# Optimization experiments

Hardware: AMD Instinct MI355X
Metric: run time of the kernel (lower is better)

The kernel has to match this reference:

```python
import jax, jax.numpy as jnp
import numpy as np

E, H, BLOCK = 1024, 64, 2048

def setup_inputs() -> dict:
    key = jax.random.key(0)
    kx, kk, kq, kv = jax.random.split(key, 4)
    s = 1.0 / np.sqrt(E)
    return {
        "x": jax.random.normal(kx, (16, 2048, E), dtype=jnp.float32),
        "Wk": jax.random.uniform(kk, (E, H), jnp.float32, -s, s),
        "Wq": jax.random.uniform(kq, (E, H), jnp.float32, -s, s),
        "Wv": jax.random.uniform(kv, (E, H), jnp.float32, -s, s),
    }

def reference(x, Wk, Wq, Wv):
    B, T, C = x.shape
    k = x @ Wk  # [B,T,H]
    q = x @ Wq
    v = x @ Wv
    scale = jnp.asarray(H, x.dtype) ** -0.5
    wei = jnp.einsum("bth,bsh->bts", q, k) * scale  # [B,T,T]
    causal = jnp.tril(jnp.ones((T, T), dtype=bool))
    wei = jnp.where(causal, wei, -jnp.inf)
    wei = jax.nn.softmax(wei, axis=-1)
    # dropout is identity in eval mode
    return jnp.einsum("bts,bsh->bth", wei, v)
```

## Files before the change

### kernel.cpp

```cpp
#include <hip/hip_runtime.h>


typedef __bf16 bf16x8 __attribute__((ext_vector_type(8)));
typedef __bf16 bf16x4 __attribute__((ext_vector_type(4)));
typedef float f32x4 __attribute__((ext_vector_type(4)));

constexpr int kE = 1024;
constexpr int kH = 64;
constexpr int kT = 2048;
constexpr int kB = 16;
constexpr int kM = kB * kT;
constexpr float kQScale = 0.125f * 1.44269504088896340736f;

#define MFMA16(a, b, c) __builtin_amdgcn_mfma_f32_16x16x32_bf16((a), (b), (c), 0, 0, 0)

__device__ __forceinline__ void gl_lds16(const void* g, void* l) {
    __builtin_amdgcn_global_load_lds(
        (const __attribute__((address_space(1))) void*)g,
        (__attribute__((address_space(3))) void*)l, 16, 0, 0);
}

__global__ __launch_bounds__(256)
void prep_w(const float* __restrict__ Wq, const float* __restrict__ Wk,
            const float* __restrict__ Wv, __bf16* __restrict__ WbT)
{
    __shared__ float tl[64][65];
    const int mat = blockIdx.x >> 4;
    const int k0 = (blockIdx.x & 15) * 64;
    const float* src = (mat == 0) ? Wq : (mat == 1) ? Wk : Wv;

    const int t = threadIdx.x;
    const int kr = t >> 2;
    const int cg = (t & 3) * 16;
    #pragma unroll
    for (int i = 0; i < 4; ++i) {
        float4 v = *(const float4*)&src[(size_t)(k0 + kr) * kH + cg + 4 * i];
        tl[cg + 4 * i + 0][kr] = v.x;
        tl[cg + 4 * i + 1][kr] = v.y;
        tl[cg + 4 * i + 2][kr] = v.z;
        tl[cg + 4 * i + 3][kr] = v.w;
    }
    __syncthreads();
    const int nl = t >> 2;
    const int kg = (t & 3) * 16;
    bf16x8 o0, o1;
    #pragma unroll
    for (int j = 0; j < 8; ++j) {
        o0[j] = (__bf16)tl[nl][kg + j];
        o1[j] = (__bf16)tl[nl][kg + 8 + j];
    }
    *(bf16x8*)&WbT[(size_t)(mat * 64 + nl) * kE + k0 + kg] = o0;
    *(bf16x8*)&WbT[(size_t)(mat * 64 + nl) * kE + k0 + kg + 8] = o1;
}

__global__ __launch_bounds__(256)
void qkv(const float* __restrict__ x, const __bf16* __restrict__ WbT,
         __bf16* __restrict__ qo, __bf16* __restrict__ ko, __bf16* __restrict__ vT)
{
    __shared__ __align__(16) char Ab[2][8192];
    __shared__ __align__(16) char Bb[2][24576];

    const int t = threadIdx.x;
    const int lane = t & 63;
    const int w = t >> 6;
    const int l15 = lane & 15;
    const int Q = lane >> 4;
    const int row0 = blockIdx.x * 64;

    f32x4 acc[4][3];
    #pragma unroll
    for (int mt = 0; mt < 4; ++mt)
        #pragma unroll
        for (int nt = 0; nt < 3; ++nt) acc[mt][nt] = (f32x4){0.f, 0.f, 0.f, 0.f};

    auto stageB = [&](int p, int k0) {
        #pragma unroll
        for (int i = 0; i < 6; ++i) {
            const int n = (w * 6 + i) * 8 + (lane >> 3);
            const int g = (lane & 7) ^ (lane >> 3);
            gl_lds16(&WbT[(size_t)n * kE + k0 + g * 8],
                     &Bb[p][(w * 6 + i) * 1024]);
        }
    };

    float4 ar[4];
    auto loadA = [&](int k0) {
        #pragma unroll
        for (int j = 0; j < 4; ++j) {
            const int row = w * 16 + j * 4 + (lane >> 4);
            ar[j] = *(const float4*)&x[(size_t)(row0 + row) * kE + k0 + l15 * 4];
        }
    };
    auto writeA = [&](int p) {
        #pragma unroll
        for (int j = 0; j < 4; ++j) {
            const int r = w * 16 + j * 4 + (lane >> 4);
            bf16x4 pk;
            pk[0] = (__bf16)ar[j].x; pk[1] = (__bf16)ar[j].y;
            pk[2] = (__bf16)ar[j].z; pk[3] = (__bf16)ar[j].w;
            *(bf16x4*)&Ab[p][r * 128 + (((l15 >> 1) ^ (r & 7)) * 16) + (l15 & 1) * 8] = pk;
        }
    };

    loadA(0);
    stageB(0, 0);
    writeA(0);
    __syncthreads();

    for (int c = 0; c < 16; ++c) {
        const int p = c & 1;
        if (c < 15) {
            loadA((c + 1) * 64);
            stageB(1 - p, (c + 1) * 64);
        }

        #pragma unroll
        for (int ks = 0; ks < 2; ++ks) {
            bf16x8 a4[4];
            #pragma unroll
            for (int mt = 0; mt < 4; ++mt) {
                const int row = mt * 16 + l15;
                a4[mt] = *(const bf16x8*)
                    &Ab[p][row * 128 + (((ks * 4 + Q) ^ (l15 & 7)) * 16)];
            }
            #pragma unroll
            for (int nt = 0; nt < 3; ++nt) {
                const int n = w * 48 + nt * 16 + l15;
                bf16x8 b = *(const bf16x8*)&Bb[p][n * 128 + (((ks * 4 + Q) ^ (l15 & 7)) * 16)];
                #pragma unroll
                for (int mt = 0; mt < 4; ++mt)
                    acc[mt][nt] = MFMA16(a4[mt], b, acc[mt][nt]);
            }
        }

        if (c < 15) writeA(1 - p);
        __syncthreads();
    }

    const int batch = row0 >> 11;
    const int tr0 = row0 & 2047;
    #pragma unroll
    for (int nt = 0; nt < 3; ++nt) {
        const int col0 = w * 48 + nt * 16;
        const int mat = col0 >> 6;
        const int c = (col0 & 63) + l15;
        if (mat == 2) {
            #pragma unroll
            for (int mt = 0; mt < 4; ++mt) {
                const int trow = tr0 + mt * 16 + Q * 4;
                bf16x4 pk;
                #pragma unroll
                for (int r = 0; r < 4; ++r) pk[r] = (__bf16)acc[mt][nt][r];
                *(bf16x4*)&vT[((size_t)batch * kH + c) * kT + trow] = pk;
            }
        } else {
            __bf16* dst = (mat == 0) ? qo : ko;
            const float sc_ = (mat == 0) ? kQScale : 1.0f;
            #pragma unroll
            for (int mt = 0; mt < 4; ++mt)
                #pragma unroll
                for (int r = 0; r < 4; ++r) {
                    const size_t row = row0 + mt * 16 + Q * 4 + r;
                    dst[row * kH + c] = (__bf16)(acc[mt][nt][r] * sc_);
                }
        }
    }
}

__global__ __launch_bounds__(256, 2)
void attn(const __bf16* __restrict__ qm, const __bf16* __restrict__ km,
          const __bf16* __restrict__ vT, float* __restrict__ out)
{
    __shared__ __align__(16) char Kb[2][8192];
    __shared__ __align__(16) char Vb[2][8192];
    __shared__ __align__(16) __bf16 Ps[4][16][72];

    const int tid = threadIdx.x;
    const int lane = tid & 63;
    const int w = tid >> 6;
    const int l15 = lane & 15;
    const int Q = lane >> 4;

    const int xcd  = blockIdx.x & 7;
    const int slot = blockIdx.x >> 3;
    const int batch = xcd + ((slot & 1) << 3);
    const int tt = (slot & 1) ? (31 - (slot >> 1)) : (slot >> 1);
    const int q16 = tt * 4 + w;
    const int qrow = q16 * 16 + l15;
    const int last = tt;

    const __bf16* qb = qm + (size_t)batch * kT * kH;
    const __bf16* kb = km + (size_t)batch * kT * kH;
    const __bf16* vb = vT + (size_t)batch * kH * kT;

    auto stage = [&](int p, int s0) {
        #pragma unroll
        for (int i = 0; i < 2; ++i) {
            const int r = w * 16 + i * 8 + (lane >> 3);
            const int g = (lane & 7) ^ (lane >> 3);
            gl_lds16(&kb[(size_t)(s0 + r) * kH + g * 8],
                     &Kb[p][(w * 2 + i) * 1024]);
            gl_lds16(&vb[(size_t)r * kT + s0 + g * 8],
                     &Vb[p][(w * 2 + i) * 1024]);
        }
    };

    bf16x8 aq[2];
    aq[0] = *(const bf16x8*)&qb[(size_t)qrow * kH + Q * 8];
    aq[1] = *(const bf16x8*)&qb[(size_t)qrow * kH + 32 + Q * 8];

    f32x4 O[4];
    #pragma unroll
    for (int i = 0; i < 4; ++i) O[i] = (f32x4){0.f, 0.f, 0.f, 0.f};
    float m_ = -3.0e38f, l_ = 0.f;

    stage(0, 0);
    __syncthreads();

    for (int kt = 0; kt <= last; ++kt) {
        const int p = kt & 1;

        bf16x8 kf[8], vf[8];
        #pragma unroll
        for (int ks = 0; ks < 2; ++ks)
            #pragma unroll
            for (int nt = 0; nt < 4; ++nt)
                kf[ks * 4 + nt] = *(const bf16x8*)
                    &Kb[p][(nt * 16 + l15) * 128 + (((ks * 4 + Q) ^ (l15 & 7)) * 16)];
        #pragma unroll
        for (int ht = 0; ht < 4; ++ht)
            #pragma unroll
            for (int ss = 0; ss < 2; ++ss)
                vf[ht * 2 + ss] = *(const bf16x8*)
                    &Vb[p][(ht * 16 + l15) * 128 + (((ss * 4 + Q) ^ (l15 & 7)) * 16)];
        asm volatile("s_waitcnt lgkmcnt(0)" ::: "memory");

        if (kt < last) stage(1 - p, (kt + 1) * 64);

        f32x4 sacc[4];
        #pragma unroll
        for (int nt = 0; nt < 4; ++nt) sacc[nt] = (f32x4){0.f, 0.f, 0.f, 0.f};
        #pragma unroll
        for (int ks = 0; ks < 2; ++ks)
            #pragma unroll
            for (int nt = 0; nt < 4; ++nt)
                sacc[nt] = MFMA16(kf[ks * 4 + nt], aq[ks], sacc[nt]);

        if (kt == last) {
            const int s0 = kt * 64;
            #pragma unroll
            for (int nt = 0; nt < 4; ++nt)
                #pragma unroll
                for (int r = 0; r < 4; ++r)
                    if (s0 + nt * 16 + Q * 4 + r > qrow) sacc[nt][r] = -3.0e38f;
        }

        float mx = sacc[0][0];
        #pragma unroll
        for (int nt = 0; nt < 4; ++nt)
            #pragma unroll
            for (int r = 0; r < 4; ++r) mx = fmaxf(mx, sacc[nt][r]);
        mx = fmaxf(mx, __shfl_xor(mx, 16));
        mx = fmaxf(mx, __shfl_xor(mx, 32));
        const float mnew = fmaxf(m_, mx);
        const float alpha = __builtin_amdgcn_exp2f(m_ - mnew);
        float rs = 0.f;
        #pragma unroll
        for (int nt = 0; nt < 4; ++nt)
            #pragma unroll
            for (int r = 0; r < 4; ++r) {
                const float pv = __builtin_amdgcn_exp2f(sacc[nt][r] - mnew);
                sacc[nt][r] = pv;
                rs += pv;
            }
        rs += __shfl_xor(rs, 16);
        rs += __shfl_xor(rs, 32);
        l_ = l_ * alpha + rs;
        m_ = mnew;
        #pragma unroll
        for (int ht = 0; ht < 4; ++ht) O[ht] *= alpha;

        #pragma unroll
        for (int nt = 0; nt < 4; ++nt) {
            bf16x4 pk;
            #pragma unroll
            for (int r = 0; r < 4; ++r) pk[r] = (__bf16)sacc[nt][r];
            *(bf16x4*)&Ps[w][l15][nt * 16 + Q * 4] = pk;
        }
        bf16x8 pb0 = *(const bf16x8*)&Ps[w][l15][Q * 8];
        bf16x8 pb1 = *(const bf16x8*)&Ps[w][l15][32 + Q * 8];

        #pragma unroll
        for (int ht = 0; ht < 4; ++ht) {
            O[ht] = MFMA16(vf[ht * 2 + 0], pb0, O[ht]);
            O[ht] = MFMA16(vf[ht * 2 + 1], pb1, O[ht]);
        }

        __syncthreads();
    }

    const float inv = 1.0f / l_;
    float* orow = out + ((size_t)batch * kT + qrow) * kH;
    #pragma unroll
    for (int ht = 0; ht < 4; ++ht) {
        float4 o4;
        o4.x = O[ht][0] * inv; o4.y = O[ht][1] * inv;
        o4.z = O[ht][2] * inv; o4.w = O[ht][3] * inv;
        *(float4*)&orow[ht * 16 + Q * 4] = o4;
    }
}

extern "C" void kernel_launch(void* const* d_in, const int* in_sizes, int n_in,
                              void* d_out, int out_size, void* d_ws, size_t ws_size,
                              hipStream_t stream)
{
    (void)in_sizes; (void)n_in; (void)out_size; (void)ws_size;
    const float* x  = (const float*)d_in[0];
    const float* Wk = (const float*)d_in[1];
    const float* Wq = (const float*)d_in[2];
    const float* Wv = (const float*)d_in[3];

    __bf16* WbT  = (__bf16*)d_ws;
    __bf16* qb   = WbT + (size_t)192 * kE;
    __bf16* kbuf = qb + (size_t)kM * kH;
    __bf16* vT   = kbuf + (size_t)kM * kH;

    prep_w<<<48, 256, 0, stream>>>(Wq, Wk, Wv, WbT);
    qkv<<<kM / 64, 256, 0, stream>>>(x, WbT, qb, kbuf, vT);
    attn<<<512, 256, 0, stream>>>(qb, kbuf, vT, (float*)d_out);
}
```

Before: 243.8 us.

## Process two 16-row query tiles per wave in attention with 2-wave blocks

The attention kernel now launches 128 threads (2 waves) per block instead of 4, and each wave handles two 16-row query sub-tiles. The K/V fragments loaded from LDS are reused across both sub-tiles, which halves LDS fragment reads per query row, and each wave stages twice as many K/V rows. In exchange it doubles per-wave accumulator and Q registers and serialises the softmax of the two sub-tiles. There are also fewer waves per CU to hide latency.

```diff
diff --git a/kernel.cpp b/kernel.cpp
--- a/kernel.cpp
+++ b/kernel.cpp
@@ -167,13 +167,13 @@
     }
 }
 
-__global__ __launch_bounds__(256, 2)
+__global__ __launch_bounds__(128, 2)
 void attn(const __bf16* __restrict__ qm, const __bf16* __restrict__ km,
           const __bf16* __restrict__ vT, float* __restrict__ out)
 {
     __shared__ __align__(16) char Kb[2][8192];
     __shared__ __align__(16) char Vb[2][8192];
-    __shared__ __align__(16) __bf16 Ps[4][16][72];
+    __shared__ __align__(16) __bf16 Ps[2][16][72];
 
     const int tid = threadIdx.x;
     const int lane = tid & 63;
@@ -185,8 +185,6 @@
     const int slot = blockIdx.x >> 3;
     const int batch = xcd + ((slot & 1) << 3);
     const int tt = (slot & 1) ? (31 - (slot >> 1)) : (slot >> 1);
-    const int q16 = tt * 4 + w;
-    const int qrow = q16 * 16 + l15;
     const int last = tt;
 
     const __bf16* qb = qm + (size_t)batch * kT * kH;
@@ -195,24 +193,32 @@
 
     auto stage = [&](int p, int s0) {
         #pragma unroll
-        for (int i = 0; i < 2; ++i) {
-            const int r = w * 16 + i * 8 + (lane >> 3);
+        for (int i = 0; i < 4; ++i) {
+            const int r = w * 32 + i * 8 + (lane >> 3);
             const int g = (lane & 7) ^ (lane >> 3);
             gl_lds16(&kb[(size_t)(s0 + r) * kH + g * 8],
-                     &Kb[p][(w * 2 + i) * 1024]);
+                     &Kb[p][(w * 4 + i) * 1024]);
             gl_lds16(&vb[(size_t)r * kT + s0 + g * 8],
-                     &Vb[p][(w * 2 + i) * 1024]);
+                     &Vb[p][(w * 4 + i) * 1024]);
         }
     };
 
-    bf16x8 aq[2];
-    aq[0] = *(const bf16x8*)&qb[(size_t)qrow * kH + Q * 8];
-    aq[1] = *(const bf16x8*)&qb[(size_t)qrow * kH + 32 + Q * 8];
-
-    f32x4 O[4];
-    #pragma unroll
-    for (int i = 0; i < 4; ++i) O[i] = (f32x4){0.f, 0.f, 0.f, 0.f};
-    float m_ = -3.0e38f, l_ = 0.f;
+    int qrow[2];
+    bf16x8 aq[2][2];
+    #pragma unroll
+    for (int s = 0; s < 2; ++s) {
+        qrow[s] = (tt * 4 + 2 * w + s) * 16 + l15;
+        aq[s][0] = *(const bf16x8*)&qb[(size_t)qrow[s] * kH + Q * 8];
+        aq[s][1] = *(const bf16x8*)&qb[(size_t)qrow[s] * kH + 32 + Q * 8];
+    }
+
+    f32x4 O[2][4];
+    #pragma unroll
+    for (int s = 0; s < 2; ++s)
+        #pragma unroll
+        for (int i = 0; i < 4; ++i) O[s][i] = (f32x4){0.f, 0.f, 0.f, 0.f};
+    float m_[2] = {-3.0e38f, -3.0e38f};
+    float l_[2] = {0.f, 0.f};
 
     stage(0, 0);
     __syncthreads();
@@ -237,76 +243,82 @@
 
         if (kt < last) stage(1 - p, (kt + 1) * 64);
 
-        f32x4 sacc[4];
-        #pragma unroll
-        for (int nt = 0; nt < 4; ++nt) sacc[nt] = (f32x4){0.f, 0.f, 0.f, 0.f};
-        #pragma unroll
-        for (int ks = 0; ks < 2; ++ks)
+        #pragma unroll
+        for (int s = 0; s < 2; ++s) {
+            f32x4 sacc[4];
+            #pragma unroll
+            for (int nt = 0; nt < 4; ++nt) sacc[nt] = (f32x4){0.f, 0.f, 0.f, 0.f};
+            #pragma unroll
+            for (int ks = 0; ks < 2; ++ks)
+                #pragma unroll
+                for (int nt = 0; nt < 4; ++nt)
+                    sacc[nt] = MFMA16(kf[ks * 4 + nt], aq[s][ks], sacc[nt]);
+
+            if (kt == last) {
+                const int s0 = kt * 64;
+                #pragma unroll
+                for (int nt = 0; nt < 4; ++nt)
+                    #pragma unroll
+                    for (int r = 0; r < 4; ++r)
+                        if (s0 + nt * 16 + Q * 4 + r > qrow[s]) sacc[nt][r] = -3.0e38f;
+            }
+
+            float mx = sacc[0][0];
             #pragma unroll
             for (int nt = 0; nt < 4; ++nt)
-                sacc[nt] = MFMA16(kf[ks * 4 + nt], aq[ks], sacc[nt]);
-
-        if (kt == last) {
-            const int s0 = kt * 64;
+                #pragma unroll
+                for (int r = 0; r < 4; ++r) mx = fmaxf(mx, sacc[nt][r]);
+            mx = fmaxf(mx, __shfl_xor(mx, 16));
+            mx = fmaxf(mx, __shfl_xor(mx, 32));
+            const float mnew = fmaxf(m_[s], mx);
+            const float alpha = __builtin_amdgcn_exp2f(m_[s] - mnew);
+            float rs = 0.f;
             #pragma unroll
             for (int nt = 0; nt < 4; ++nt)
                 #pragma unroll
-                for (int r = 0; r < 4; ++r)
-                    if (s0 + nt * 16 + Q * 4 + r > qrow) sacc[nt][r] = -3.0e38f;
-        }
-
-        float mx = sacc[0][0];
-        #pragma unroll
-        for (int nt = 0; nt < 4; ++nt)
-            #pragma unroll
-            for (int r = 0; r < 4; ++r) mx = fmaxf(mx, sacc[nt][r]);
-        mx = fmaxf(mx, __shfl_xor(mx, 16));
-        mx = fmaxf(mx, __shfl_xor(mx, 32));
-        const float mnew = fmaxf(m_, mx);
-        const float alpha = __builtin_amdgcn_exp2f(m_ - mnew);
-        float rs = 0.f;
-        #pragma unroll
-        for (int nt = 0; nt < 4; ++nt)
-            #pragma unroll
-            for (int r = 0; r < 4; ++r) {
-                const float pv = __builtin_amdgcn_exp2f(sacc[nt][r] - mnew);
-                sacc[nt][r] = pv;
-                rs += pv;
-            }
-        rs += __shfl_xor(rs, 16);
-        rs += __shfl_xor(rs, 32);
-        l_ = l_ * alpha + rs;
-        m_ = mnew;
-        #pragma unroll
-        for (int ht = 0; ht < 4; ++ht) O[ht] *= alpha;
-
-        #pragma unroll
-        for (int nt = 0; nt < 4; ++nt) {
-            bf16x4 pk;
-            #pragma unroll
-            for (int r = 0; r < 4; ++r) pk[r] = (__bf16)sacc[nt][r];
-            *(bf16x4*)&Ps[w][l15][nt * 16 + Q * 4] = pk;
-        }
-        bf16x8 pb0 = *(const bf16x8*)&Ps[w][l15][Q * 8];
-        bf16x8 pb1 = *(const bf16x8*)&Ps[w][l15][32 + Q * 8];
-
+                for (int r = 0; r < 4; ++r) {
+                    const float pv = __builtin_amdgcn_exp2f(sacc[nt][r] - mnew);
+                    sacc[nt][r] = pv;
+                    rs += pv;
+                }
+            rs += __shfl_xor(rs, 16);
+            rs += __shfl_xor(rs, 32);
+            l_[s] = l_[s] * alpha + rs;
+            m_[s] = mnew;
+            #pragma unroll
+            for (int ht = 0; ht < 4; ++ht) O[s][ht] *= alpha;
+
+            #pragma unroll
+            for (int nt = 0; nt < 4; ++nt) {
+                bf16x4 pk;
+                #pragma unroll
+                for (int r = 0; r < 4; ++r) pk[r] = (__bf16)sacc[nt][r];
+                *(bf16x4*)&Ps[w][l15][nt * 16 + Q * 4] = pk;
+            }
+            bf16x8 pb0 = *(const bf16x8*)&Ps[w][l15][Q * 8];
+            bf16x8 pb1 = *(const bf16x8*)&Ps[w][l15][32 + Q * 8];
+
+            #pragma unroll
+            for (int ht = 0; ht < 4; ++ht) {
+                O[s][ht] = MFMA16(vf[ht * 2 + 0], pb0, O[s][ht]);
+                O[s][ht] = MFMA16(vf[ht * 2 + 1], pb1, O[s][ht]);
+            }
+        }
+
+        __syncthreads();
+    }
+
+    #pragma unroll
+    for (int s = 0; s < 2; ++s) {
+        const float inv = 1.0f / l_[s];
+        float* orow = out + ((size_t)batch * kT + qrow[s]) * kH;
         #pragma unroll
         for (int ht = 0; ht < 4; ++ht) {
-            O[ht] = MFMA16(vf[ht * 2 + 0], pb0, O[ht]);
-            O[ht] = MFMA16(vf[ht * 2 + 1], pb1, O[ht]);
-        }
-
-        __syncthreads();
-    }
-
-    const float inv = 1.0f / l_;
-    float* orow = out + ((size_t)batch * kT + qrow) * kH;
-    #pragma unroll
-    for (int ht = 0; ht < 4; ++ht) {
-        float4 o4;
-        o4.x = O[ht][0] * inv; o4.y = O[ht][1] * inv;
-        o4.z = O[ht][2] * inv; o4.w = O[ht][3] * inv;
-        *(float4*)&orow[ht * 16 + Q * 4] = o4;
+            float4 o4;
+            o4.x = O[s][ht][0] * inv; o4.y = O[s][ht][1] * inv;
+            o4.z = O[s][ht][2] * inv; o4.w = O[s][ht][3] * inv;
+            *(float4*)&orow[ht * 16 + Q * 4] = o4;
+        }
     }
 }
 
@@ -327,5 +339,5 @@
 
     prep_w<<<48, 256, 0, stream>>>(Wq, Wk, Wv, WbT);
     qkv<<<kM / 64, 256, 0, stream>>>(x, WbT, qb, kbuf, vT);
-    attn<<<512, 256, 0, stream>>>(qb, kbuf, vT, (float*)d_out);
-}
+    attn<<<512, 128, 0, stream>>>(qb, kbuf, vT, (float*)d_out);
+}
```

Result: slower. 253.9 us (+4.2%).

## Feed P to PV MFMA from registers using 16x16x16 bf16 instructions

Applied to the files above, without the earlier changes.

Drops the per-wave LDS round-trip for the softmax probabilities. The S accumulator layout is fed directly as the B operand of 16x16x16 bf16 MFMAs, and the V fragments are reloaded as 4-element pieces to match. The row max and sum reductions are also rebalanced into trees. The cost is twice as many smaller MFMA instructions, which run at lower throughput per instruction than the 16x16x32 variant, plus more, smaller LDS reads for V.

```diff
diff --git a/kernel.cpp b/kernel.cpp
--- a/kernel.cpp
+++ b/kernel.cpp
@@ -3,6 +3,7 @@
 
 typedef __bf16 bf16x8 __attribute__((ext_vector_type(8)));
 typedef __bf16 bf16x4 __attribute__((ext_vector_type(4)));
+typedef short s16x4 __attribute__((ext_vector_type(4)));
 typedef float f32x4 __attribute__((ext_vector_type(4)));
 
 constexpr int kE = 1024;
@@ -13,6 +14,8 @@
 constexpr float kQScale = 0.125f * 1.44269504088896340736f;
 
 #define MFMA16(a, b, c) __builtin_amdgcn_mfma_f32_16x16x32_bf16((a), (b), (c), 0, 0, 0)
+#define MFMA16K16(a, b, c) \
+    __builtin_amdgcn_mfma_f32_16x16x16bf16_1k((a), (b), (c), 0, 0, 0)
 
 __device__ __forceinline__ void gl_lds16(const void* g, void* l) {
     __builtin_amdgcn_global_load_lds(
@@ -173,7 +176,6 @@
 {
     __shared__ __align__(16) char Kb[2][8192];
     __shared__ __align__(16) char Vb[2][8192];
-    __shared__ __align__(16) __bf16 Ps[4][16][72];
 
     const int tid = threadIdx.x;
     const int lane = tid & 63;
@@ -220,7 +222,8 @@
     for (int kt = 0; kt <= last; ++kt) {
         const int p = kt & 1;
 
-        bf16x8 kf[8], vf[8];
+        bf16x8 kf[8];
+        bf16x4 vf4[4][4];
         #pragma unroll
         for (int ks = 0; ks < 2; ++ks)
             #pragma unroll
@@ -230,9 +233,10 @@
         #pragma unroll
         for (int ht = 0; ht < 4; ++ht)
             #pragma unroll
-            for (int ss = 0; ss < 2; ++ss)
-                vf[ht * 2 + ss] = *(const bf16x8*)
-                    &Vb[p][(ht * 16 + l15) * 128 + (((ss * 4 + Q) ^ (l15 & 7)) * 16)];
+            for (int nt = 0; nt < 4; ++nt)
+                vf4[ht][nt] = *(const bf16x4*)
+                    &Vb[p][(ht * 16 + l15) * 128
+                           + (((2 * nt + (Q >> 1)) ^ (l15 & 7)) * 16) + (Q & 1) * 8];
         asm volatile("s_waitcnt lgkmcnt(0)" ::: "memory");
 
         if (kt < last) stage(1 - p, (kt + 1) * 64);
@@ -255,24 +259,24 @@
                     if (s0 + nt * 16 + Q * 4 + r > qrow) sacc[nt][r] = -3.0e38f;
         }
 
-        float mx = sacc[0][0];
+        float mnt[4], snt[4];
         #pragma unroll
         for (int nt = 0; nt < 4; ++nt)
-            #pragma unroll
-            for (int r = 0; r < 4; ++r) mx = fmaxf(mx, sacc[nt][r]);
+            mnt[nt] = fmaxf(fmaxf(sacc[nt][0], sacc[nt][1]),
+                            fmaxf(sacc[nt][2], sacc[nt][3]));
+        float mx = fmaxf(fmaxf(mnt[0], mnt[1]), fmaxf(mnt[2], mnt[3]));
         mx = fmaxf(mx, __shfl_xor(mx, 16));
         mx = fmaxf(mx, __shfl_xor(mx, 32));
         const float mnew = fmaxf(m_, mx);
         const float alpha = __builtin_amdgcn_exp2f(m_ - mnew);
-        float rs = 0.f;
-        #pragma unroll
-        for (int nt = 0; nt < 4; ++nt)
-            #pragma unroll
-            for (int r = 0; r < 4; ++r) {
-                const float pv = __builtin_amdgcn_exp2f(sacc[nt][r] - mnew);
-                sacc[nt][r] = pv;
-                rs += pv;
-            }
+        #pragma unroll
+        for (int nt = 0; nt < 4; ++nt) {
+            #pragma unroll
+            for (int r = 0; r < 4; ++r)
+                sacc[nt][r] = __builtin_amdgcn_exp2f(sacc[nt][r] - mnew);
+            snt[nt] = (sacc[nt][0] + sacc[nt][1]) + (sacc[nt][2] + sacc[nt][3]);
+        }
+        float rs = (snt[0] + snt[1]) + (snt[2] + snt[3]);
         rs += __shfl_xor(rs, 16);
         rs += __shfl_xor(rs, 32);
         l_ = l_ * alpha + rs;
@@ -280,21 +284,21 @@
         #pragma unroll
         for (int ht = 0; ht < 4; ++ht) O[ht] *= alpha;
 
+        s16x4 pb[4];
         #pragma unroll
         for (int nt = 0; nt < 4; ++nt) {
             bf16x4 pk;
             #pragma unroll
             for (int r = 0; r < 4; ++r) pk[r] = (__bf16)sacc[nt][r];
-            *(bf16x4*)&Ps[w][l15][nt * 16 + Q * 4] = pk;
-        }
-        bf16x8 pb0 = *(const bf16x8*)&Ps[w][l15][Q * 8];
-        bf16x8 pb1 = *(const bf16x8*)&Ps[w][l15][32 + Q * 8];
-
-        #pragma unroll
-        for (int ht = 0; ht < 4; ++ht) {
-            O[ht] = MFMA16(vf[ht * 2 + 0], pb0, O[ht]);
-            O[ht] = MFMA16(vf[ht * 2 + 1], pb1, O[ht]);
-        }
+            pb[nt] = __builtin_bit_cast(s16x4, pk);
+        }
+
+        #pragma unroll
+        for (int ht = 0; ht < 4; ++ht)
+            #pragma unroll
+            for (int nt = 0; nt < 4; ++nt)
+                O[ht] = MFMA16K16(__builtin_bit_cast(s16x4, vf4[ht][nt]),
+                                  pb[nt], O[ht]);
 
         __syncthreads();
     }
```

After: 250.0 us. 2.6% more time.
